# Optimization experiments

Hardware: AMD Instinct MI355X
Metric: run time of the kernel (lower is better)

The kernel has to match this reference:

```python
import jax, jax.numpy as jnp
import numpy as np

B, T, H, NH, HD = 2, 2048, 2048, 16, 128


def setup_inputs() -> dict:
    key = jax.random.key(0)
    k1, k2, k3 = jax.random.split(key, 3)
    hidden_states = jax.random.normal(k1, (B, T, H), dtype=jnp.float32)
    w_qkv = jax.random.normal(k2, (3 * H, H), dtype=jnp.float32) * (1.0 / np.sqrt(H))
    w_out = jax.random.normal(k3, (H, H), dtype=jnp.float32) * (1.0 / np.sqrt(H))
    return {"hidden_states": hidden_states, "w_qkv": w_qkv, "w_out": w_out}


def reference(hidden_states, w_qkv, w_out):
    scale = 1.0 / np.sqrt(HD)
    # qkv projection: torch Linear is x @ W.T with W [out, in]
    qkv = jnp.einsum('bth,oh->bto', hidden_states, w_qkv)  # [B, T, 3H]
    q, k, v = jnp.split(qkv, 3, axis=2)
    # [B, NH, T, HD]
    q = q.reshape(B, T, NH, HD).transpose(0, 2, 1, 3)
    k = k.reshape(B, T, NH, HD).transpose(0, 2, 1, 3)
    v = v.reshape(B, T, NH, HD).transpose(0, 2, 1, 3)
    scores = jnp.einsum('bhqd,bhkd->bhqk', q, k) * scale  # [B, NH, T, T]
    mask = jnp.tril(jnp.ones((T, T), dtype=bool))  # causal
    scores = jnp.where(mask[None, None], scores, -jnp.inf)
    probs = jax.nn.softmax(scores, axis=-1)
    attn = jnp.einsum('bhqk,bhkd->bhqd', probs, v)  # [B, NH, T, HD]
    attn = attn.transpose(0, 2, 1, 3).reshape(B, T, H)
    out = jnp.einsum('bth,oh->bto', attn, w_out)
    return out
```

## Files before the change

### kernel.cpp

```cpp
#include <hip/hip_runtime.h>
#include <cstdint>
#include <cstddef>

typedef _Float16 f16x8 __attribute__((ext_vector_type(8)));
typedef _Float16 f16x4 __attribute__((ext_vector_type(4)));
typedef float    f32x4 __attribute__((ext_vector_type(4)));
typedef unsigned short ushort_t;

#define LOG2E 1.4426950408889634f

constexpr int BATCH = 2;
constexpr int TSEQ  = 2048;
constexpr int HID   = 2048;
constexpr int NH    = 16;
constexpr int HD    = 128;
constexpr int GK    = 2048;
constexpr int NKT   = GK / 64;

__device__ inline f32x4 mfma16(f16x8 a, f16x8 b, f32x4 c) {
    return __builtin_amdgcn_mfma_f32_16x16x32_f16(a, b, c, 0, 0, 0);
}

__device__ inline void async_copy16(const void* src, void* dst_lds) {
    __builtin_amdgcn_global_load_lds(
        (const __attribute__((address_space(1))) uint32_t*)src,
        (__attribute__((address_space(3))) uint32_t*)dst_lds, 16, 0, 0);
}

__device__ inline uint32_t pkrtz(float a, float b) {
    union { decltype(__builtin_amdgcn_cvt_pkrtz(0.f, 0.f)) h; uint32_t u; } cv;
    cv.h = __builtin_amdgcn_cvt_pkrtz(a, b);
    return cv.u;
}

__global__ __launch_bounds__(256)
void cast_all(const float4* __restrict__ hs, const float4* __restrict__ wqkv,
              const float4* __restrict__ wout, f16x4* __restrict__ hs_h,
              f16x4* __restrict__ wqkv_h, f16x4* __restrict__ wout_h,
              int n_hs, int n_wqkv, int n_wout) {
    int i = blockIdx.x * 256 + threadIdx.x;
    const float4* src; f16x4* dst; int j;
    if (i < n_hs)                 { src = hs;   dst = hs_h;   j = i; }
    else if (i < n_hs + n_wqkv)   { src = wqkv; dst = wqkv_h; j = i - n_hs; }
    else if (i < n_hs + n_wqkv + n_wout) { src = wout; dst = wout_h; j = i - n_hs - n_wqkv; }
    else return;
    float4 v = src[j];
    f16x4 o = { (_Float16)v.x, (_Float16)v.y, (_Float16)v.z, (_Float16)v.w };
    dst[j] = o;
}

template <int MODE>
__global__ __launch_bounds__(512, 2)
void gemm_big(const _Float16* __restrict__ A, const _Float16* __restrict__ B,
              float* __restrict__ C, _Float16* __restrict__ Qo,
              _Float16* __restrict__ Ko, _Float16* __restrict__ Vo, int NB) {
    __shared__ __align__(16) _Float16 As[3][256 * 64];
    __shared__ __align__(16) _Float16 Bs[3][128 * 64];

    const int tid  = threadIdx.x;
    const int lane = tid & 63;
    const int w    = tid >> 6;
    const int l15  = lane & 15;
    const int lq   = lane >> 4;
    const int wr   = w >> 1, wc = w & 1;

    const int bid = (int)blockIdx.x;
    const int cpx = (int)gridDim.x >> 3;
    const int swz = (bid & 7) * cpx + (bid >> 3);
    const int bn  = swz % NB, bm = swz / NB;
    const int m0  = bm * 256, n0 = bn * 128;

    const _Float16* Ab = A + (size_t)m0 * GK;
    const _Float16* Bb = B + (size_t)n0 * GK;

    auto stage = [&](int t, int b) {
        const int k0 = t * 64;
        #pragma unroll
        for (int it = 0; it < 4; ++it) {
            const int slot = it * 512 + tid;
            const int row = slot >> 3, c16 = slot & 7;
            const int srcb = c16 ^ (row & 7);
            async_copy16(Ab + (size_t)row * GK + k0 + srcb * 8,
                         (char*)As[b] + slot * 16);
        }
        #pragma unroll
        for (int it = 0; it < 2; ++it) {
            const int slot = it * 512 + tid;
            const int row = slot >> 3, c16 = slot & 7;
            const int srcb = c16 ^ (row & 7);
            async_copy16(Bb + (size_t)row * GK + k0 + srcb * 8,
                         (char*)Bs[b] + slot * 16);
        }
    };

    f32x4 acc[4][4] = {};

    stage(0, 0);
    stage(1, 1);

    for (int t = 0; t < NKT; ++t) {
        if (t + 1 < NKT) asm volatile("s_waitcnt vmcnt(6)" ::: "memory");
        else             asm volatile("s_waitcnt vmcnt(0)" ::: "memory");
        __builtin_amdgcn_s_barrier();
        __builtin_amdgcn_sched_barrier(0);

        const char* At_ = (const char*)As[t % 3];
        const char* Bt_ = (const char*)Bs[t % 3];

        f16x8 af[4][2], bff[4][2];
        #pragma unroll
        for (int i = 0; i < 4; ++i)
            #pragma unroll
            for (int kk = 0; kk < 2; ++kk) {
                const int ra = wr * 64 + i * 16 + l15;
                af[i][kk]  = *(const f16x8*)(At_ + ra * 128 + (((kk * 4 + lq) ^ (ra & 7)) << 4));
                const int rb = wc * 64 + i * 16 + l15;
                bff[i][kk] = *(const f16x8*)(Bt_ + rb * 128 + (((kk * 4 + lq) ^ (rb & 7)) << 4));
            }

        if (t + 2 < NKT) stage(t + 2, (t + 2) % 3);

        __builtin_amdgcn_s_setprio(1);
        #pragma unroll
        for (int kk = 0; kk < 2; ++kk)
            #pragma unroll
            for (int i = 0; i < 4; ++i)
                #pragma unroll
                for (int j = 0; j < 4; ++j)
                    acc[i][j] = mfma16(af[i][kk], bff[j][kk], acc[i][j]);
        __builtin_amdgcn_s_setprio(0);
    }

    if (MODE == 0) {
        #pragma unroll
        for (int j = 0; j < 4; ++j) {
            const int ncol = n0 + wc * 64 + j * 16 + l15;
            const int which = ncol >> 11;
            const int oo = ncol & 2047;
            const int head = oo >> 7;
            const int d = oo & 127;
            _Float16* dst = (which == 0) ? Qo : (which == 1) ? Ko : Vo;
            const float scl = (which == 0) ? 0.08838834764831845f : 1.0f;
            #pragma unroll
            for (int i = 0; i < 4; ++i) {
                #pragma unroll
                for (int r = 0; r < 4; ++r) {
                    const int m = m0 + wr * 64 + i * 16 + lq * 4 + r;
                    const int b = m >> 11, tt = m & 2047;
                    dst[((size_t)(b * NH + head) * TSEQ + tt) * HD + d] =
                        (_Float16)(acc[i][j][r] * scl);
                }
            }
        }
    } else {
        #pragma unroll
        for (int i = 0; i < 4; ++i)
            #pragma unroll
            for (int j = 0; j < 4; ++j)
                #pragma unroll
                for (int r = 0; r < 4; ++r) {
                    const int m = m0 + wr * 64 + i * 16 + lq * 4 + r;
                    const int n = n0 + wc * 64 + j * 16 + l15;
                    C[(size_t)m * HID + n] = acc[i][j][r];
                }
    }
}

template <int MODE>
__global__ __launch_bounds__(256, 2)
void gemm_small(const _Float16* __restrict__ A, const _Float16* __restrict__ B,
                float* __restrict__ C, int NB) {
    __shared__ __align__(16) _Float16 As[2][128 * 64];
    __shared__ __align__(16) _Float16 Bs[2][128 * 64];

    const int tid  = threadIdx.x;
    const int lane = tid & 63;
    const int w    = tid >> 6;
    const int l15  = lane & 15;
    const int lq   = lane >> 4;
    const int wr   = w >> 1, wc = w & 1;

    const int bid = (int)blockIdx.x;
    const int cpx = (int)gridDim.x >> 3;
    const int swz = (bid & 7) * cpx + (bid >> 3);
    const int bn  = swz % NB, bm = swz / NB;
    const int m0  = bm * 128, n0 = bn * 128;

    const _Float16* Ab = A + (size_t)m0 * GK;
    const _Float16* Bb = B + (size_t)n0 * GK;

    auto stage = [&](int t, int b) {
        const int k0 = t * 64;
        #pragma unroll
        for (int it = 0; it < 4; ++it) {
            const int slot = it * 256 + tid;
            const int row = slot >> 3, c16 = slot & 7;
            const int srcb = c16 ^ (row & 7);
            async_copy16(Ab + (size_t)row * GK + k0 + srcb * 8,
                         (char*)As[b] + slot * 16);
        }
        #pragma unroll
        for (int it = 0; it < 4; ++it) {
            const int slot = it * 256 + tid;
            const int row = slot >> 3, c16 = slot & 7;
            const int srcb = c16 ^ (row & 7);
            async_copy16(Bb + (size_t)row * GK + k0 + srcb * 8,
                         (char*)Bs[b] + slot * 16);
        }
    };

    f32x4 acc[4][4] = {};

    stage(0, 0);
    stage(1, 1);

    for (int t = 0; t < NKT; ++t) {
        const int cur = t & 1;
        if (t + 1 < NKT) asm volatile("s_waitcnt vmcnt(8)" ::: "memory");
        else             asm volatile("s_waitcnt vmcnt(0)" ::: "memory");
        __builtin_amdgcn_s_barrier();
        __builtin_amdgcn_sched_barrier(0);

        const char* At_ = (const char*)As[cur];
        const char* Bt_ = (const char*)Bs[cur];

        f16x8 af[4][2], bff[4][2];
        #pragma unroll
        for (int i = 0; i < 4; ++i)
            #pragma unroll
            for (int kk = 0; kk < 2; ++kk) {
                const int ra = wr * 64 + i * 16 + l15;
                af[i][kk]  = *(const f16x8*)(At_ + ra * 128 + (((kk * 4 + lq) ^ (ra & 7)) << 4));
                const int rb = wc * 64 + i * 16 + l15;
                bff[i][kk] = *(const f16x8*)(Bt_ + rb * 128 + (((kk * 4 + lq) ^ (rb & 7)) << 4));
            }
        asm volatile("s_waitcnt lgkmcnt(0)" ::: "memory");
        __builtin_amdgcn_sched_barrier(0);
        __builtin_amdgcn_s_barrier();
        __builtin_amdgcn_sched_barrier(0);

        if (t + 2 < NKT) stage(t + 2, cur);

        __builtin_amdgcn_s_setprio(1);
        #pragma unroll
        for (int kk = 0; kk < 2; ++kk)
            #pragma unroll
            for (int i = 0; i < 4; ++i)
                #pragma unroll
                for (int j = 0; j < 4; ++j)
                    acc[i][j] = mfma16(af[i][kk], bff[j][kk], acc[i][j]);
        __builtin_amdgcn_s_setprio(0);
    }

    #pragma unroll
    for (int i = 0; i < 4; ++i)
        #pragma unroll
        for (int j = 0; j < 4; ++j)
            #pragma unroll
            for (int r = 0; r < 4; ++r) {
                const int m = m0 + wr * 64 + i * 16 + lq * 4 + r;
                const int n = n0 + wc * 64 + j * 16 + l15;
                C[(size_t)m * HID + n] = acc[i][j][r];
            }
}

__global__ __launch_bounds__(256)
void attn_fwd(const _Float16* __restrict__ Q, const _Float16* __restrict__ K,
              const _Float16* __restrict__ V, _Float16* __restrict__ O) {
    __shared__ __align__(16) char Ks[64 * 256];
    __shared__ __align__(16) char Vt[128 * 128];

    const int tid  = threadIdx.x;
    const int lane = tid & 63;
    const int w    = tid >> 6;
    const int l15  = lane & 15;
    const int lq   = lane >> 4;
    const int lq1  = lq >> 1;
    const int laneA = l15 + ((lane & 16) << 1);
    const int laneB = laneA + 16;

    const int bh   = (int)blockIdx.x & 31;
    const int pair = (int)blockIdx.x >> 5;
    const int b = bh >> 4, h = bh & 15;

    const size_t base = (size_t)bh * TSEQ * HD;
    const _Float16* Qp = Q + base;
    const _Float16* Kp = K + base;
    const _Float16* Vp = V + base;

    uint4 vv[4];
    auto loadV = [&](int t) {
        const int row = tid & 63;
        #pragma unroll
        for (int it = 0; it < 4; ++it) {
            const int c8 = w * 4 + it;
            vv[it] = *(const uint4*)(Vp + (size_t)(t * 64 + row) * HD + c8 * 8);
        }
    };
    auto stageK = [&](int t) {
        #pragma unroll
        for (int it = 0; it < 4; ++it) {
            const int slot = it * 256 + tid;
            const int row = slot >> 4, c16 = slot & 15;
            const int srcb = c16 ^ (row & 7);
            async_copy16(Kp + (size_t)(t * 64 + row) * HD + srcb * 8, Ks + slot * 16);
        }
    };
    auto writeV = [&]() {
        const int row = tid & 63;
        #pragma unroll
        for (int it = 0; it < 4; ++it) {
            const int c8 = w * 4 + it;
            const uint32_t wrd[4] = {vv[it].x, vv[it].y, vv[it].z, vv[it].w};
            #pragma unroll
            for (int p2 = 0; p2 < 4; ++p2) {
                const int d0 = c8 * 8 + p2 * 2, d1 = d0 + 1;
                int b0 = d0 * 128 + row * 2; b0 ^= (d0 & 7) << 4;
                int b1 = d1 * 128 + row * 2; b1 ^= (d1 & 7) << 4;
                *(ushort_t*)(Vt + b0) = (ushort_t)(wrd[p2] & 0xffffu);
                *(ushort_t*)(Vt + b1) = (ushort_t)(wrd[p2] >> 16);
            }
        }
    };

    for (int phase = 0; phase < 2; ++phase) {
        const int qt = phase ? pair : (31 - pair);
        const int q0 = qt * 64;
        const int NT = qt + 1;

        if (phase) __syncthreads();

        const int qrow = q0 + w * 16 + l15;
        f16x8 qf[4];
        #pragma unroll
        for (int ks = 0; ks < 4; ++ks)
            qf[ks] = *(const f16x8*)(Qp + (size_t)qrow * HD + ks * 32 + lq * 8);

        f32x4 o[8] = {};
        float m_run = -1e30f;
        float osum  = 0.0f;

        stageK(0);
        loadV(0);

        for (int t = 0; t < NT; ++t) {
            writeV();
            __syncthreads();
            if (t + 1 < NT) loadV(t + 1);

            const int kv0 = t * 64;
            f32x4 s[4] = {};
            __builtin_amdgcn_s_setprio(1);
            #pragma unroll
            for (int ks = 0; ks < 4; ++ks) {
                #pragma unroll
                for (int nf = 0; nf < 4; ++nf) {
                    const int r   = nf * 16 + l15;
                    const int blk = (ks * 4 + lq) ^ (r & 7);
                    const f16x8 kf = *(const f16x8*)(Ks + r * 256 + blk * 16);
                    s[nf] = mfma16(kf, qf[ks], s[nf]);
                }
            }
            __builtin_amdgcn_s_setprio(0);

            if (kv0 + 63 > q0 + w * 16) {
                const int q_lane = q0 + w * 16 + l15;
                #pragma unroll
                for (int nf = 0; nf < 4; ++nf) {
                    #pragma unroll
                    for (int r = 0; r < 4; ++r) {
                        const int kv = kv0 + nf * 16 + lq * 4 + r;
                        if (kv > q_lane) s[nf][r] = -1e30f;
                    }
                }
            }

            float lmax = -1e30f;
            #pragma unroll
            for (int nf = 0; nf < 4; ++nf)
                lmax = fmaxf(lmax, fmaxf(fmaxf(s[nf][0], s[nf][1]),
                                         fmaxf(s[nf][2], s[nf][3])));
            if (__any(lmax > m_run + 5.0f)) {
                float v = lmax;
                v = fmaxf(v, __shfl_xor(v, 16));
                v = fmaxf(v, __shfl_xor(v, 32));
                const float mn = fmaxf(m_run, v);
                const float alpha = __builtin_exp2f((m_run - mn) * LOG2E);
                m_run = mn;
                osum *= alpha;
                float aq[4];
                #pragma unroll
                for (int r = 0; r < 4; ++r)
                    aq[r] = __shfl(alpha, lq * 4 + r);
                #pragma unroll
                for (int df = 0; df < 8; ++df)
                    #pragma unroll
                    for (int r = 0; r < 4; ++r)
                        o[df][r] *= aq[r];
            }

            uint32_t pk[4][2];
            float psum = 0.0f;
            #pragma unroll
            for (int nf = 0; nf < 4; ++nf) {
                #pragma unroll
                for (int hh = 0; hh < 2; ++hh) {
                    const float pa = __builtin_exp2f((s[nf][2 * hh]     - m_run) * LOG2E);
                    const float pb = __builtin_exp2f((s[nf][2 * hh + 1] - m_run) * LOG2E);
                    psum += pa + pb;
                    pk[nf][hh] = pkrtz(pa, pb);
                }
            }
            osum += psum;

            f16x8 pf[2];
            #pragma unroll
            for (int ks2 = 0; ks2 < 2; ++ks2) {
                union { uint32_t u[4]; f16x8 v; } pu;
                const uint32_t a0n0 = (uint32_t)__shfl((int)pk[2 * ks2][0],     laneA);
                const uint32_t a0n1 = (uint32_t)__shfl((int)pk[2 * ks2 + 1][0], laneA);
                const uint32_t a1n0 = (uint32_t)__shfl((int)pk[2 * ks2][1],     laneA);
                const uint32_t a1n1 = (uint32_t)__shfl((int)pk[2 * ks2 + 1][1], laneA);
                const uint32_t b0n0 = (uint32_t)__shfl((int)pk[2 * ks2][0],     laneB);
                const uint32_t b0n1 = (uint32_t)__shfl((int)pk[2 * ks2 + 1][0], laneB);
                const uint32_t b1n0 = (uint32_t)__shfl((int)pk[2 * ks2][1],     laneB);
                const uint32_t b1n1 = (uint32_t)__shfl((int)pk[2 * ks2 + 1][1], laneB);
                pu.u[0] = lq1 ? a0n1 : a0n0;
                pu.u[1] = lq1 ? a1n1 : a1n0;
                pu.u[2] = lq1 ? b0n1 : b0n0;
                pu.u[3] = lq1 ? b1n1 : b1n0;
                pf[ks2] = pu.v;
            }

            __builtin_amdgcn_s_setprio(1);
            #pragma unroll
            for (int ks2 = 0; ks2 < 2; ++ks2) {
                #pragma unroll
                for (int df = 0; df < 8; ++df) {
                    const int vr   = df * 16 + l15;
                    const int vblk = (ks2 * 4 + lq) ^ (vr & 7);
                    const f16x8 vf = *(const f16x8*)(Vt + vr * 128 + vblk * 16);
                    o[df] = mfma16(pf[ks2], vf, o[df]);
                }
            }
            __builtin_amdgcn_s_setprio(0);

            if (t + 1 < NT) {
                __syncthreads();
                stageK(t + 1);
            }
        }

        float tot = osum;
        tot += __shfl_xor(tot, 16);
        tot += __shfl_xor(tot, 32);
        const float rl = 1.0f / tot;
        float rlq[4];
        #pragma unroll
        for (int r = 0; r < 4; ++r)
            rlq[r] = __shfl(rl, lq * 4 + r);

        #pragma unroll
        for (int df = 0; df < 8; ++df) {
            #pragma unroll
            for (int r = 0; r < 4; ++r) {
                const int qg = q0 + w * 16 + lq * 4 + r;
                const int dg = df * 16 + l15;
                O[((size_t)(b * TSEQ + qg)) * HID + h * HD + dg] =
                    (_Float16)(o[df][r] * rlq[r]);
            }
        }
    }
}

extern "C" void kernel_launch(void* const* d_in, const int* in_sizes, int n_in,
                              void* d_out, int out_size, void* d_ws, size_t ws_size,
                              hipStream_t stream) {
    (void)in_sizes; (void)n_in; (void)out_size; (void)ws_size;
    const float* hs   = (const float*)d_in[0];
    const float* wqkv = (const float*)d_in[1];
    const float* wout = (const float*)d_in[2];

    char* ws = (char*)d_ws;
    size_t off = 0;
    _Float16* hs_h   = (_Float16*)(ws + off); off += (size_t)BATCH * TSEQ * HID * 2;
    _Float16* wqkv_h = (_Float16*)(ws + off); off += (size_t)3 * HID * HID * 2;
    _Float16* wout_h = (_Float16*)(ws + off); off += (size_t)HID * HID * 2;
    _Float16* Qh     = (_Float16*)(ws + off); off += (size_t)BATCH * NH * TSEQ * HD * 2;
    _Float16* Kh     = (_Float16*)(ws + off); off += (size_t)BATCH * NH * TSEQ * HD * 2;
    _Float16* Vh     = (_Float16*)(ws + off); off += (size_t)BATCH * NH * TSEQ * HD * 2;
    _Float16* At     = (_Float16*)(ws + off); off += (size_t)BATCH * TSEQ * HID * 2;

    const int n4_hs   = BATCH * TSEQ * HID / 4;
    const int n4_wqkv = 3 * HID * HID / 4;
    const int n4_wout = HID * HID / 4;
    const int n4_all  = n4_hs + n4_wqkv + n4_wout;
    cast_all<<<dim3((n4_all + 255) / 256), dim3(256), 0, stream>>>(
        (const float4*)hs, (const float4*)wqkv, (const float4*)wout,
        (f16x4*)hs_h, (f16x4*)wqkv_h, (f16x4*)wout_h, n4_hs, n4_wqkv, n4_wout);

    gemm_big<0><<<dim3(768), dim3(512), 0, stream>>>(
        hs_h, wqkv_h, nullptr, Qh, Kh, Vh, 48);

    attn_fwd<<<dim3(512), dim3(256), 0, stream>>>(Qh, Kh, Vh, At);

    gemm_small<1><<<dim3(512), dim3(256), 0, stream>>>(
        At, wout_h, (float*)d_out, 16);
}
```

Before: 263.5 us.

## Enlarge QKV GEMM tile to 256x256 with double-buffered phased LDS refill

The QKV projection GEMM now uses 256x256 output tiles per block, with 8 waves laid out 2x4 and 128x64 per wave, in a grid of 384 blocks. LDS staging drops from a 3-stage to a 2-stage buffer. Each k-step is split into phases, and the next B and A tiles are refilled into the just-consumed buffer after intermediate barriers. The larger tile raises arithmetic intensity and cuts global reloads. In exchange it adds more accumulator registers, likely one block per CU, extra barriers per k-step, and fewer blocks than the CU count allows for balanced waves.

```diff
diff --git a/kernel.cpp b/kernel.cpp
--- a/kernel.cpp
+++ b/kernel.cpp
@@ -49,31 +49,41 @@
     dst[j] = o;
 }
 
-template <int MODE>
-__global__ __launch_bounds__(512, 2)
-void gemm_big(const _Float16* __restrict__ A, const _Float16* __restrict__ B,
-              float* __restrict__ C, _Float16* __restrict__ Qo,
-              _Float16* __restrict__ Ko, _Float16* __restrict__ Vo, int NB) {
-    __shared__ __align__(16) _Float16 As[3][256 * 64];
-    __shared__ __align__(16) _Float16 Bs[3][128 * 64];
+__global__ __launch_bounds__(512)
+void gemm_qkv(const _Float16* __restrict__ A, const _Float16* __restrict__ B,
+              _Float16* __restrict__ Qo, _Float16* __restrict__ Ko,
+              _Float16* __restrict__ Vo) {
+    __shared__ __align__(16) _Float16 As[2][256 * 64];
+    __shared__ __align__(16) _Float16 Bs[2][256 * 64];
 
     const int tid  = threadIdx.x;
     const int lane = tid & 63;
     const int w    = tid >> 6;
     const int l15  = lane & 15;
     const int lq   = lane >> 4;
-    const int wr   = w >> 1, wc = w & 1;
+    const int wr   = w >> 2;
+    const int wc   = w & 3;
 
     const int bid = (int)blockIdx.x;
-    const int cpx = (int)gridDim.x >> 3;
-    const int swz = (bid & 7) * cpx + (bid >> 3);
-    const int bn  = swz % NB, bm = swz / NB;
-    const int m0  = bm * 256, n0 = bn * 128;
+    const int swz = (bid & 7) * 48 + (bid >> 3);
+    const int bn  = swz % 24, bm = swz / 24;
+    const int m0  = bm * 256, n0 = bn * 256;
 
     const _Float16* Ab = A + (size_t)m0 * GK;
     const _Float16* Bb = B + (size_t)n0 * GK;
 
-    auto stage = [&](int t, int b) {
+    auto stageB = [&](int t, int c) {
+        const int k0 = t * 64;
+        #pragma unroll
+        for (int it = 0; it < 4; ++it) {
+            const int slot = it * 512 + tid;
+            const int row = slot >> 3, c16 = slot & 7;
+            const int srcb = c16 ^ (row & 7);
+            async_copy16(Bb + (size_t)row * GK + k0 + srcb * 8,
+                         (char*)Bs[c] + slot * 16);
+        }
+    };
+    auto stageA = [&](int t, int c) {
         const int k0 = t * 64;
         #pragma unroll
         for (int it = 0; it < 4; ++it) {
@@ -81,88 +91,120 @@
             const int row = slot >> 3, c16 = slot & 7;
             const int srcb = c16 ^ (row & 7);
             async_copy16(Ab + (size_t)row * GK + k0 + srcb * 8,
-                         (char*)As[b] + slot * 16);
-        }
-        #pragma unroll
-        for (int it = 0; it < 2; ++it) {
-            const int slot = it * 512 + tid;
-            const int row = slot >> 3, c16 = slot & 7;
-            const int srcb = c16 ^ (row & 7);
-            async_copy16(Bb + (size_t)row * GK + k0 + srcb * 8,
-                         (char*)Bs[b] + slot * 16);
+                         (char*)As[c] + slot * 16);
         }
     };
 
-    f32x4 acc[4][4] = {};
-
-    stage(0, 0);
-    stage(1, 1);
+    f32x4 acc[8][4] = {};
+
+    stageB(0, 0); stageA(0, 0);
+    stageB(1, 1); stageA(1, 1);
 
     for (int t = 0; t < NKT; ++t) {
-        if (t + 1 < NKT) asm volatile("s_waitcnt vmcnt(6)" ::: "memory");
+        const int c = t & 1;
+        if (t + 1 < NKT) asm volatile("s_waitcnt vmcnt(8)" ::: "memory");
         else             asm volatile("s_waitcnt vmcnt(0)" ::: "memory");
         __builtin_amdgcn_s_barrier();
         __builtin_amdgcn_sched_barrier(0);
 
-        const char* At_ = (const char*)As[t % 3];
-        const char* Bt_ = (const char*)Bs[t % 3];
-
-        f16x8 af[4][2], bff[4][2];
-        #pragma unroll
-        for (int i = 0; i < 4; ++i)
+        const char* At_ = (const char*)As[c];
+        const char* Bt_ = (const char*)Bs[c];
+
+        f16x8 bfr[4][2];
+        #pragma unroll
+        for (int j = 0; j < 4; ++j)
             #pragma unroll
             for (int kk = 0; kk < 2; ++kk) {
-                const int ra = wr * 64 + i * 16 + l15;
-                af[i][kk]  = *(const f16x8*)(At_ + ra * 128 + (((kk * 4 + lq) ^ (ra & 7)) << 4));
-                const int rb = wc * 64 + i * 16 + l15;
-                bff[i][kk] = *(const f16x8*)(Bt_ + rb * 128 + (((kk * 4 + lq) ^ (rb & 7)) << 4));
-            }
-
-        if (t + 2 < NKT) stage(t + 2, (t + 2) % 3);
+                const int rb = wc * 64 + j * 16 + l15;
+                bfr[j][kk] = *(const f16x8*)(Bt_ + rb * 128 + (((kk * 4 + lq) ^ (rb & 7)) << 4));
+            }
+        f16x8 af[2][2];
+        #pragma unroll
+        for (int i = 0; i < 2; ++i)
+            #pragma unroll
+            for (int kk = 0; kk < 2; ++kk) {
+                const int ra = wr * 128 + i * 16 + l15;
+                af[i][kk] = *(const f16x8*)(At_ + ra * 128 + (((kk * 4 + lq) ^ (ra & 7)) << 4));
+            }
+        asm volatile("s_waitcnt lgkmcnt(0)" ::: "memory");
+        __builtin_amdgcn_sched_barrier(0);
+        __builtin_amdgcn_s_barrier();
+        __builtin_amdgcn_sched_barrier(0);
+        if (t + 2 < NKT) stageB(t + 2, c);
 
         __builtin_amdgcn_s_setprio(1);
         #pragma unroll
         for (int kk = 0; kk < 2; ++kk)
             #pragma unroll
-            for (int i = 0; i < 4; ++i)
+            for (int i = 0; i < 2; ++i)
                 #pragma unroll
                 for (int j = 0; j < 4; ++j)
-                    acc[i][j] = mfma16(af[i][kk], bff[j][kk], acc[i][j]);
+                    acc[i][j] = mfma16(af[i][kk], bfr[j][kk], acc[i][j]);
+        __builtin_amdgcn_s_setprio(0);
+
+        #pragma unroll
+        for (int ph = 1; ph <= 2; ++ph) {
+            #pragma unroll
+            for (int i = 0; i < 2; ++i)
+                #pragma unroll
+                for (int kk = 0; kk < 2; ++kk) {
+                    const int ra = wr * 128 + (ph * 2 + i) * 16 + l15;
+                    af[i][kk] = *(const f16x8*)(At_ + ra * 128 + (((kk * 4 + lq) ^ (ra & 7)) << 4));
+                }
+            __builtin_amdgcn_s_setprio(1);
+            #pragma unroll
+            for (int kk = 0; kk < 2; ++kk)
+                #pragma unroll
+                for (int i = 0; i < 2; ++i)
+                    #pragma unroll
+                    for (int j = 0; j < 4; ++j)
+                        acc[ph * 2 + i][j] = mfma16(af[i][kk], bfr[j][kk], acc[ph * 2 + i][j]);
+            __builtin_amdgcn_s_setprio(0);
+        }
+
+        #pragma unroll
+        for (int i = 0; i < 2; ++i)
+            #pragma unroll
+            for (int kk = 0; kk < 2; ++kk) {
+                const int ra = wr * 128 + (6 + i) * 16 + l15;
+                af[i][kk] = *(const f16x8*)(At_ + ra * 128 + (((kk * 4 + lq) ^ (ra & 7)) << 4));
+            }
+        asm volatile("s_waitcnt lgkmcnt(0)" ::: "memory");
+        __builtin_amdgcn_sched_barrier(0);
+        __builtin_amdgcn_s_barrier();
+        __builtin_amdgcn_sched_barrier(0);
+        if (t + 2 < NKT) stageA(t + 2, c);
+
+        __builtin_amdgcn_s_setprio(1);
+        #pragma unroll
+        for (int kk = 0; kk < 2; ++kk)
+            #pragma unroll
+            for (int i = 0; i < 2; ++i)
+                #pragma unroll
+                for (int j = 0; j < 4; ++j)
+                    acc[6 + i][j] = mfma16(af[i][kk], bfr[j][kk], acc[6 + i][j]);
         __builtin_amdgcn_s_setprio(0);
     }
 
-    if (MODE == 0) {
-        #pragma unroll
-        for (int j = 0; j < 4; ++j) {
-            const int ncol = n0 + wc * 64 + j * 16 + l15;
-            const int which = ncol >> 11;
-            const int oo = ncol & 2047;
-            const int head = oo >> 7;
-            const int d = oo & 127;
-            _Float16* dst = (which == 0) ? Qo : (which == 1) ? Ko : Vo;
-            const float scl = (which == 0) ? 0.08838834764831845f : 1.0f;
-            #pragma unroll
-            for (int i = 0; i < 4; ++i) {
-                #pragma unroll
-                for (int r = 0; r < 4; ++r) {
-                    const int m = m0 + wr * 64 + i * 16 + lq * 4 + r;
-                    const int b = m >> 11, tt = m & 2047;
-                    dst[((size_t)(b * NH + head) * TSEQ + tt) * HD + d] =
-                        (_Float16)(acc[i][j][r] * scl);
-                }
-            }
-        }
-    } else {
-        #pragma unroll
-        for (int i = 0; i < 4; ++i)
-            #pragma unroll
-            for (int j = 0; j < 4; ++j)
-                #pragma unroll
-                for (int r = 0; r < 4; ++r) {
-                    const int m = m0 + wr * 64 + i * 16 + lq * 4 + r;
-                    const int n = n0 + wc * 64 + j * 16 + l15;
-                    C[(size_t)m * HID + n] = acc[i][j][r];
-                }
+    #pragma unroll
+    for (int j = 0; j < 4; ++j) {
+        const int ncol = n0 + wc * 64 + j * 16 + l15;
+        const int which = ncol >> 11;
+        const int oo = ncol & 2047;
+        const int head = oo >> 7;
+        const int d = oo & 127;
+        _Float16* dst = (which == 0) ? Qo : (which == 1) ? Ko : Vo;
+        const float scl = (which == 0) ? 0.08838834764831845f : 1.0f;
+        #pragma unroll
+        for (int i = 0; i < 8; ++i) {
+            #pragma unroll
+            for (int r = 0; r < 4; ++r) {
+                const int m = m0 + wr * 128 + i * 16 + lq * 4 + r;
+                const int b = m >> 11, tt = m & 2047;
+                dst[((size_t)(b * NH + head) * TSEQ + tt) * HD + d] =
+                    (_Float16)(acc[i][j][r] * scl);
+            }
+        }
     }
 }
 
@@ -499,8 +541,7 @@
         (const float4*)hs, (const float4*)wqkv, (const float4*)wout,
         (f16x4*)hs_h, (f16x4*)wqkv_h, (f16x4*)wout_h, n4_hs, n4_wqkv, n4_wout);
 
-    gemm_big<0><<<dim3(768), dim3(512), 0, stream>>>(
-        hs_h, wqkv_h, nullptr, Qh, Kh, Vh, 48);
+    gemm_qkv<<<dim3(384), dim3(512), 0, stream>>>(hs_h, wqkv_h, Qh, Kh, Vh);
 
     attn_fwd<<<dim3(512), dim3(256), 0, stream>>>(Qh, Kh, Vh, At);
 
```

Measured after the change: 291.2 us. 10.5% more time.
